# Kernel tuning notes

Measured on AMD Instinct MI355X. Metric: run time of the kernel, lower is better.

Reference implementation:

```python
import jax, jax.numpy as jnp
import numpy as np
from jax import lax

# TT-conv configuration (matches init_kwargs)
M = (4, 8, 8)        # in_c_modes, prod = 256
O = (4, 8, 8)        # out_c_modes, prod = 256
R = (16, 16, 16, 1)  # ranks with trailing 1 appended as in the module
B, H, W = 8, 64, 64
IN_C = int(np.prod(M))


def setup_inputs() -> dict:
    key = jax.random.key(0)
    ks = jax.random.split(key, 6)
    X = jax.random.normal(ks[0], (B, IN_C, H, W), jnp.float32)
    conv_w = jax.random.normal(ks[1], (R[0], 1, 3, 3), jnp.float32) * 0.3
    conv_b = jax.random.normal(ks[2], (R[0],), jnp.float32) * 0.05
    def xavier(k, shape):
        fan_in, fan_out = shape[1], shape[0]
        std = (2.0 / (fan_in + fan_out)) ** 0.5
        return jax.random.normal(k, shape, jnp.float32) * std
    core1 = xavier(ks[3], (O[0] * R[1], R[0] * M[0]))  # (64, 64)
    core2 = xavier(ks[4], (O[1] * R[2], R[1] * M[1]))  # (128, 128)
    core3 = xavier(ks[5], (O[2] * R[3], R[2] * M[2]))  # (8, 128)
    return {"X": X, "conv_w": conv_w, "conv_b": conv_b,
            "core1": core1, "core2": core2, "core3": core3}


def reference(X, conv_w, conv_b, core1, core2, core3):
    b, in_c, h, w = X.shape
    # core0: depth-agnostic 1->r0 conv applied per input channel
    y = lax.conv_general_dilated(
        X.reshape(-1, 1, h, w), conv_w,
        window_strides=(1, 1), padding=((1, 1), (1, 1)),
        dimension_numbers=("NCHW", "OIHW", "NCHW"))
    y = y + conv_b[None, :, None, None]          # (B*in_c, r0, h, w)
    hh, ww = y.shape[-2:]
    # (B, m1, m2, m3, r0, h, w): in_c factored row-major, m1 most significant
    y = y.reshape(b, M[0], M[1], M[2], R[0], hh, ww)
    # TT cores reshaped (o_i, r_{i+1}, r_i, m_i)
    G1 = core1.reshape(O[0], R[1], R[0], M[0])
    G2 = core2.reshape(O[1], R[2], R[1], M[1])
    G3 = core3.reshape(O[2], R[3], R[2], M[2])
    # Full TT contraction chain collapsed into one einsum; s (=r3) has size 1.
    out = jnp.einsum("bijkrhw,auri,cvuj,dsvk->bacdhw",
                     y, G1, G2, G3, optimize=True)
    # channel order (o1, o2, o3) with o3 fastest, as in the torch module
    return out.reshape(b, O[0] * O[1] * O[2], hh, ww)
```

## Files before the change

kernel.cpp:

```cpp
#include <hip/hip_runtime.h>
#include <hip/hip_bf16.h>
#include <stdint.h>

typedef __attribute__((ext_vector_type(8))) short short8;
typedef __attribute__((ext_vector_type(4))) float f32x4;

#define XP_BYTES   17842176
#define XP_PAD     1024
#define OFF_W9     (XP_BYTES + XP_PAD)
#define W9_BYTES   (8*9*256*32*2)
#define OFF_BIAS   (OFF_W9 + W9_BYTES)

__device__ __forceinline__ short f2bf(float f) {
  __hip_bfloat16 h = __float2bfloat16(f);
  return *reinterpret_cast<short*>(&h);
}

__device__ __forceinline__ void gl_lds16(const void* g, void* l) {
  __builtin_amdgcn_global_load_lds(
      (const __attribute__((address_space(1))) void*)g,
      (__attribute__((address_space(3))) void*)l, 16, 0, 0);
}

__global__ void k_weights(const float* __restrict__ core1,
                          const float* __restrict__ core2,
                          const float* __restrict__ core3,
                          const float* __restrict__ convw,
                          const float* __restrict__ convb,
                          short* __restrict__ W9, float* __restrict__ bias) {
  __shared__ float H2s[1024];
  __shared__ float red[256];
  const int o = blockIdx.x, c = threadIdx.x;
  const int a = o >> 6, c2 = (o >> 3) & 7, d = o & 7;
#pragma unroll
  for (int p = 0; p < 4; ++p) {
    int idx = c + (p << 8);
    int k = idx & 7, j = (idx >> 3) & 7, u = idx >> 6;
    float s = 0.f;
#pragma unroll
    for (int v = 0; v < 16; ++v)
      s += core2[(c2 * 16 + v) * 128 + u * 8 + j] * core3[d * 128 + v * 8 + k];
    H2s[idx] = s;
  }
  __syncthreads();
  const int i = c >> 6, j = (c >> 3) & 7, k = c & 7;
  float Wr[16];
#pragma unroll
  for (int r = 0; r < 16; ++r) Wr[r] = 0.f;
  for (int u = 0; u < 16; ++u) {
    float h = H2s[u * 64 + j * 8 + k];
    const float* c1 = core1 + (a * 16 + u) * 64 + i;
#pragma unroll
    for (int r = 0; r < 16; ++r) Wr[r] += c1[r * 4] * h;
  }
  const int cb = c >> 5, cl = c & 31, g = cl >> 3, pos = cl & 7;
  const int gslot = g ^ (o & 3);
#pragma unroll
  for (int t = 0; t < 9; ++t) {
    float s = 0.f;
#pragma unroll
    for (int r = 0; r < 16; ++r) s += Wr[r] * convw[r * 9 + t];
    W9[((size_t)((cb * 9 + t) * 256 + o)) * 32 + gslot * 8 + pos] = f2bf(s);
  }
  float s = 0.f;
#pragma unroll
  for (int r = 0; r < 16; ++r) s += Wr[r] * convb[r];
  red[c] = s;
  __syncthreads();
  for (int st = 128; st > 0; st >>= 1) {
    if (c < st) red[c] += red[c + st];
    __syncthreads();
  }
  if (c == 0) bias[o] = red[0];
}

__global__ void k_pad(const float* __restrict__ X, short* __restrict__ Xp) {
  const int yp = blockIdx.x, b = blockIdx.y, cb = blockIdx.z;
  const int t = threadIdx.x;
  const int x = t & 63, sub = t >> 6;
  const size_t rowg = ((size_t)((b * 8 + cb) * 66 + yp)) * 264;
  const short8 z = (short8){0, 0, 0, 0, 0, 0, 0, 0};
  if (yp == 0 || yp == 65) {
    *(short8*)(Xp + (rowg + (size_t)(x << 2) + sub) * 8) = z;
    if (x < 2)
      *(short8*)(Xp + (rowg + (size_t)((64 + x) << 2) + sub) * 8) = z;
    return;
  }
  const int y = yp - 1, xp = x + 1;
  const int gslot = sub ^ ((xp >> 1) & 3);
  const float* src = X + ((size_t)(b * 256 + cb * 32 + sub * 8) * 64 + y) * 64 + x;
  short8 v;
#pragma unroll
  for (int k = 0; k < 8; ++k) v[k] = f2bf(src[(size_t)k * 4096]);
  *(short8*)(Xp + (rowg + (size_t)(xp << 2) + gslot) * 8) = v;
  if (x < 2)
    *(short8*)(Xp + (rowg + (size_t)((x * 65) << 2) + sub) * 8) = z;
}

__global__ __launch_bounds__(512, 1) void k_gemm(
    const short* __restrict__ Xp, const short* __restrict__ W9,
    const float* __restrict__ bias, float* __restrict__ out) {
  __shared__ __align__(16) short XL[2][38400];

  const int tid  = threadIdx.x;
  const int lane = tid & 63;
  const int wv   = tid >> 6;
  const int l15  = lane & 15;
  const int gl   = lane >> 4;
  const int h0    = blockIdx.x << 4;
  const int oBase = blockIdx.y << 5;
  const int b     = blockIdx.z;
  const int r0    = wv << 1;

  int xoff[4][3];
#pragma unroll
  for (int xr = 0; xr < 4; ++xr)
#pragma unroll
    for (int dx = 0; dx < 3; ++dx)
      xoff[xr][dx] = ((r0 + xr) * 66 + l15 + dx) * 32 +
                     ((gl ^ (((l15 + dx) >> 1) & 3)) << 3);

  const int laneW = (oBase + l15) * 32 + ((gl ^ (l15 & 3)) << 3);

  f32x4 acc[2][2][4];
#pragma unroll
  for (int rr = 0; rr < 2; ++rr)
#pragma unroll
    for (int io = 0; io < 2; ++io)
#pragma unroll
      for (int ip = 0; ip < 4; ++ip)
        acc[rr][io][ip] = (f32x4){0.f, 0.f, 0.f, 0.f};

#define STAGE(CB, BUF)                                                     \
  {                                                                        \
    const size_t xb = ((size_t)(((b << 3) + (CB)) * 66 + h0) * 66) << 5;   \
    _Pragma("unroll 1")                                                    \
    for (int q = wv; q < 75; q += 8)                                       \
      gl_lds16(Xp + xb + (q << 9) + (lane << 3), &XL[BUF][q << 9]);        \
  }

  STAGE(0, 0);

  for (int cb = 0; cb < 8; ++cb) {
    const short* Wc = W9 + cb * 73728 + laneW;
    short8 af[9][2];
#pragma unroll
    for (int t = 0; t < 9; ++t)
#pragma unroll
      for (int io = 0; io < 2; ++io)
        af[t][io] = *(const short8*)&Wc[t * 8192 + (io << 9)];
    __builtin_amdgcn_sched_barrier(0);

    __syncthreads();

    if (cb < 7) STAGE(cb + 1, (cb + 1) & 1);
    __builtin_amdgcn_sched_barrier(0);

    const short* XLc = &XL[cb & 1][0];
    short8 bfr[2][4];

#define LOADS(BUF, DX, IP)                                                 \
  {                                                                        \
    _Pragma("unroll")                                                      \
    for (int xr = 0; xr < 4; ++xr)                                         \
      bfr[BUF][xr] = *(const short8*)&XLc[xoff[xr][DX] + ((IP) << 9)];     \
  }

    LOADS(0, 0, 0);
#pragma unroll
    for (int s = 0; s < 12; ++s) {
      const int dx = s >> 2, ip = s & 3, buf = s & 1;
      if (s < 11) LOADS(buf ^ 1, (s + 1) >> 2, (s + 1) & 3);
      __builtin_amdgcn_sched_barrier(0);
      __builtin_amdgcn_s_setprio(1);
#pragma unroll
      for (int dy = 0; dy < 3; ++dy) {
        const int t = dy * 3 + dx;
#pragma unroll
        for (int io = 0; io < 2; ++io) {
          acc[0][io][ip] = __builtin_amdgcn_mfma_f32_16x16x32_bf16(
              af[t][io], bfr[buf][dy], acc[0][io][ip], 0, 0, 0);
          acc[1][io][ip] = __builtin_amdgcn_mfma_f32_16x16x32_bf16(
              af[t][io], bfr[buf][dy + 1], acc[1][io][ip], 0, 0, 0);
        }
      }
      __builtin_amdgcn_s_setprio(0);
    }
#undef LOADS
  }
#undef STAGE

#pragma unroll
  for (int rr = 0; rr < 2; ++rr) {
    const int h = h0 + r0 + rr;
#pragma unroll
    for (int io = 0; io < 2; ++io) {
#pragma unroll
      for (int r = 0; r < 4; ++r) {
        const int oG = oBase + (io << 4) + (gl << 2) + r;
        const float bv = bias[oG];
        float* op = out + (((size_t)((b << 8) + oG)) << 12) + (h << 6);
#pragma unroll
        for (int ip = 0; ip < 4; ++ip)
          op[(ip << 4) + l15] = acc[rr][io][ip][r] + bv;
      }
    }
  }
}

extern "C" void kernel_launch(void* const* d_in, const int* in_sizes, int n_in,
                              void* d_out, int out_size, void* d_ws, size_t ws_size,
                              hipStream_t stream) {
  (void)in_sizes; (void)n_in; (void)out_size; (void)ws_size;
  const float* X     = (const float*)d_in[0];
  const float* convw = (const float*)d_in[1];
  const float* convb = (const float*)d_in[2];
  const float* core1 = (const float*)d_in[3];
  const float* core2 = (const float*)d_in[4];
  const float* core3 = (const float*)d_in[5];
  float* out = (float*)d_out;
  char*  ws  = (char*)d_ws;

  short* Xp   = (short*)ws;
  short* W9   = (short*)(ws + OFF_W9);
  float* bias = (float*)(ws + OFF_BIAS);

  k_weights<<<256, 256, 0, stream>>>(core1, core2, core3, convw, convb, W9, bias);
  k_pad    <<<dim3(66, 8, 8), 256, 0, stream>>>(X, Xp);
  k_gemm   <<<dim3(4, 8, 8), 512, 0, stream>>>(Xp, W9, bias, out);
}
```

Before: 135.4 us.

## Fuse weight prep, padding and GEMM into one cooperative kernel with grid sync

Merges the three launches (weight/bias folding, bf16 pad/transpose of X, and the MFMA conv-GEMM) into a single cooperative kernel of 256 blocks, separated by a grid-wide sync. This removes two kernel launch gaps and the tail of each small kernel. The pad stage now stages each row through LDS so the global stores are contiguous, and the bias reduction uses wave shuffles instead of a tree in shared memory. In exchange it depends on all 256 blocks being co-resident for the grid sync and pays the cost of the cooperative launch and the barrier.

```diff
diff --git a/kernel.cpp b/kernel.cpp
--- a/kernel.cpp
+++ b/kernel.cpp
@@ -1,6 +1,9 @@
 #include <hip/hip_runtime.h>
+#include <hip/hip_cooperative_groups.h>
 #include <hip/hip_bf16.h>
 #include <stdint.h>
+
+namespace cg = cooperative_groups;
 
 typedef __attribute__((ext_vector_type(8))) short short8;
 typedef __attribute__((ext_vector_type(4))) float f32x4;
@@ -22,94 +25,119 @@
       (__attribute__((address_space(3))) void*)l, 16, 0, 0);
 }
 
-__global__ void k_weights(const float* __restrict__ core1,
-                          const float* __restrict__ core2,
-                          const float* __restrict__ core3,
-                          const float* __restrict__ convw,
-                          const float* __restrict__ convb,
-                          short* __restrict__ W9, float* __restrict__ bias) {
-  __shared__ float H2s[1024];
-  __shared__ float red[256];
-  const int o = blockIdx.x, c = threadIdx.x;
-  const int a = o >> 6, c2 = (o >> 3) & 7, d = o & 7;
-#pragma unroll
-  for (int p = 0; p < 4; ++p) {
-    int idx = c + (p << 8);
-    int k = idx & 7, j = (idx >> 3) & 7, u = idx >> 6;
+__global__ __launch_bounds__(512, 1) void k_fused(
+    const float* __restrict__ X, const float* __restrict__ core1,
+    const float* __restrict__ core2, const float* __restrict__ core3,
+    const float* __restrict__ convw, const float* __restrict__ convb,
+    short* __restrict__ Xp, short* __restrict__ W9,
+    float* __restrict__ bias, float* __restrict__ out) {
+  __shared__ __align__(16) short SM[76800];
+  const int tid = threadIdx.x;
+  const int bid = blockIdx.x;
+
+  {
+    float* H2s = (float*)SM;
+    float* partial = H2s + 1024;
+    const int o = bid;
+    const int a = o >> 6, c2 = (o >> 3) & 7, d = o & 7;
+#pragma unroll
+    for (int p = 0; p < 2; ++p) {
+      int idx = tid + (p << 9);
+      int k = idx & 7, j = (idx >> 3) & 7, u = idx >> 6;
+      float s = 0.f;
+#pragma unroll
+      for (int v = 0; v < 16; ++v)
+        s += core2[(c2 * 16 + v) * 128 + u * 8 + j] * core3[d * 128 + v * 8 + k];
+      H2s[idx] = s;
+    }
+    __syncthreads();
     float s = 0.f;
-#pragma unroll
-    for (int v = 0; v < 16; ++v)
-      s += core2[(c2 * 16 + v) * 128 + u * 8 + j] * core3[d * 128 + v * 8 + k];
-    H2s[idx] = s;
-  }
-  __syncthreads();
-  const int i = c >> 6, j = (c >> 3) & 7, k = c & 7;
-  float Wr[16];
-#pragma unroll
-  for (int r = 0; r < 16; ++r) Wr[r] = 0.f;
-  for (int u = 0; u < 16; ++u) {
-    float h = H2s[u * 64 + j * 8 + k];
-    const float* c1 = core1 + (a * 16 + u) * 64 + i;
-#pragma unroll
-    for (int r = 0; r < 16; ++r) Wr[r] += c1[r * 4] * h;
-  }
-  const int cb = c >> 5, cl = c & 31, g = cl >> 3, pos = cl & 7;
-  const int gslot = g ^ (o & 3);
-#pragma unroll
-  for (int t = 0; t < 9; ++t) {
-    float s = 0.f;
-#pragma unroll
-    for (int r = 0; r < 16; ++r) s += Wr[r] * convw[r * 9 + t];
-    W9[((size_t)((cb * 9 + t) * 256 + o)) * 32 + gslot * 8 + pos] = f2bf(s);
-  }
-  float s = 0.f;
-#pragma unroll
-  for (int r = 0; r < 16; ++r) s += Wr[r] * convb[r];
-  red[c] = s;
-  __syncthreads();
-  for (int st = 128; st > 0; st >>= 1) {
-    if (c < st) red[c] += red[c + st];
+    if (tid < 256) {
+      const int c = tid;
+      const int i = c >> 6, j = (c >> 3) & 7, k = c & 7;
+      float Wr[16];
+#pragma unroll
+      for (int r = 0; r < 16; ++r) Wr[r] = 0.f;
+      for (int u = 0; u < 16; ++u) {
+        float h = H2s[u * 64 + j * 8 + k];
+        const float* c1 = core1 + (a * 16 + u) * 64 + i;
+#pragma unroll
+        for (int r = 0; r < 16; ++r) Wr[r] += c1[r * 4] * h;
+      }
+      const int cb = c >> 5, cl = c & 31, gg = cl >> 3, pos = cl & 7;
+      const int gslot = gg ^ (o & 3);
+#pragma unroll
+      for (int t = 0; t < 9; ++t) {
+        float sw = 0.f;
+#pragma unroll
+        for (int r = 0; r < 16; ++r) sw += Wr[r] * convw[r * 9 + t];
+        W9[((size_t)((cb * 9 + t) * 256 + o)) * 32 + gslot * 8 + pos] = f2bf(sw);
+      }
+#pragma unroll
+      for (int r = 0; r < 16; ++r) s += Wr[r] * convb[r];
+    }
+#pragma unroll
+    for (int off = 32; off; off >>= 1) s += __shfl_down(s, off);
+    if ((tid & 63) == 0 && tid < 256) partial[tid >> 6] = s;
     __syncthreads();
-  }
-  if (c == 0) bias[o] = red[0];
-}
-
-__global__ void k_pad(const float* __restrict__ X, short* __restrict__ Xp) {
-  const int yp = blockIdx.x, b = blockIdx.y, cb = blockIdx.z;
-  const int t = threadIdx.x;
-  const int x = t & 63, sub = t >> 6;
-  const size_t rowg = ((size_t)((b * 8 + cb) * 66 + yp)) * 264;
-  const short8 z = (short8){0, 0, 0, 0, 0, 0, 0, 0};
-  if (yp == 0 || yp == 65) {
-    *(short8*)(Xp + (rowg + (size_t)(x << 2) + sub) * 8) = z;
-    if (x < 2)
-      *(short8*)(Xp + (rowg + (size_t)((64 + x) << 2) + sub) * 8) = z;
-    return;
-  }
-  const int y = yp - 1, xp = x + 1;
-  const int gslot = sub ^ ((xp >> 1) & 3);
-  const float* src = X + ((size_t)(b * 256 + cb * 32 + sub * 8) * 64 + y) * 64 + x;
-  short8 v;
-#pragma unroll
-  for (int k = 0; k < 8; ++k) v[k] = f2bf(src[(size_t)k * 4096]);
-  *(short8*)(Xp + (rowg + (size_t)(xp << 2) + gslot) * 8) = v;
-  if (x < 2)
-    *(short8*)(Xp + (rowg + (size_t)((x * 65) << 2) + sub) * 8) = z;
-}
-
-__global__ __launch_bounds__(512, 1) void k_gemm(
-    const short* __restrict__ Xp, const short* __restrict__ W9,
-    const float* __restrict__ bias, float* __restrict__ out) {
-  __shared__ __align__(16) short XL[2][38400];
-
-  const int tid  = threadIdx.x;
+    if (tid == 0) bias[o] = partial[0] + partial[1] + partial[2] + partial[3];
+  }
+
+  {
+    const int team = tid >> 8, tl = tid & 255;
+    short* Ls = &SM[38400 + team * 2304];
+    const short8 z = (short8){0, 0, 0, 0, 0, 0, 0, 0};
+    if (tl < 8) {
+      const int gid = (tl < 4) ? tl : 260 + (tl - 4);
+      *(short8*)&Ls[gid * 8] = z;
+    }
+    const int x = tl & 63, sub = tl >> 6, xp = x + 1;
+    const int gslot = sub ^ ((xp >> 1) & 3);
+    for (int it = 0; it < 9; ++it) {
+      const int j = it * 512 + (bid << 1) + team;
+      const bool act = j < 4224;
+      short* rowp = nullptr;
+      bool border = false;
+      short8 v;
+      if (act) {
+        const int yp = j % 66, bc = j / 66;
+        const int b_ = bc >> 3, cb_ = bc & 7;
+        rowp = Xp + ((size_t)((b_ * 8 + cb_) * 66 + yp)) * 264 * 8;
+        border = (yp == 0) || (yp == 65);
+        if (!border) {
+          const int y = yp - 1;
+          const float* src =
+              X + ((size_t)(b_ * 256 + cb_ * 32 + sub * 8) * 64 + y) * 64 + x;
+#pragma unroll
+          for (int k = 0; k < 8; ++k) v[k] = f2bf(src[(size_t)k * 4096]);
+        }
+      }
+      __syncthreads();
+      if (act && !border) *(short8*)&Ls[(xp * 4 + gslot) * 8] = v;
+      __syncthreads();
+      if (act) {
+        if (border) {
+          *(short8*)(rowp + tl * 8) = z;
+          if (tl < 8) *(short8*)(rowp + (256 + tl) * 8) = z;
+        } else {
+          *(short8*)(rowp + tl * 8) = *(const short8*)&Ls[tl * 8];
+          if (tl < 8)
+            *(short8*)(rowp + (256 + tl) * 8) = *(const short8*)&Ls[(256 + tl) * 8];
+        }
+      }
+    }
+  }
+
+  cg::this_grid().sync();
+
+  short (*XL)[38400] = reinterpret_cast<short (*)[38400]>(SM);
   const int lane = tid & 63;
   const int wv   = tid >> 6;
   const int l15  = lane & 15;
   const int gl   = lane >> 4;
-  const int h0    = blockIdx.x << 4;
-  const int oBase = blockIdx.y << 5;
-  const int b     = blockIdx.z;
+  const int h0    = (bid & 3) << 4;
+  const int oBase = ((bid >> 2) & 7) << 5;
+  const int b     = bid >> 5;
   const int r0    = wv << 1;
 
   int xoff[4][3];
@@ -225,7 +253,9 @@
   short* W9   = (short*)(ws + OFF_W9);
   float* bias = (float*)(ws + OFF_BIAS);
 
-  k_weights<<<256, 256, 0, stream>>>(core1, core2, core3, convw, convb, W9, bias);
-  k_pad    <<<dim3(66, 8, 8), 256, 0, stream>>>(X, Xp);
-  k_gemm   <<<dim3(4, 8, 8), 512, 0, stream>>>(Xp, W9, bias, out);
-}
+  void* args[] = {(void*)&X, (void*)&core1, (void*)&core2, (void*)&core3,
+                  (void*)&convw, (void*)&convb, (void*)&Xp, (void*)&W9,
+                  (void*)&bias, (void*)&out};
+  hipLaunchCooperativeKernel((const void*)k_fused, dim3(256), dim3(512),
+                             args, 0, stream);
+}
```

Result: slower. 182.9 us (+35.1%).
